# Kernel tuning notes

Measured on AMD Instinct MI355X. Metric: run time of the kernel, lower is better.

Reference implementation:

```python
import jax, jax.numpy as jnp
import numpy as np

B, S, D, L = 4, 2048, 1024, 4  # batch, seq_len, d_model, num_layers


def setup_inputs() -> dict:
    key = jax.random.key(0)
    ks = jax.random.split(key, 6)
    w = lambda k, shape: jax.random.normal(k, shape, jnp.float32) * 0.02
    return {
        "x": jax.random.normal(ks[0], (B, S, D), jnp.float32),
        # stacked per-layer parameters [L, ...]
        "Wkqv": w(ks[1], (L, D, 3 * D)),
        "Wm1": w(ks[2], (L, D, 2 * D)), "bm1": jnp.zeros((L, 2 * D), jnp.float32),
        "Wm2": w(ks[3], (L, D, D)), "bm2": jnp.zeros((L, D), jnp.float32),
        "gn_g": jnp.ones((L, D), jnp.float32), "gn_b": jnp.zeros((L, D), jnp.float32),
        "Wf1": w(ks[4], (L, D, 2 * D)), "bf1": jnp.zeros((L, 2 * D), jnp.float32),
        "Wf2": w(ks[5], (L, 2 * D, D)), "bf2": jnp.zeros((L, D), jnp.float32),
        "ln_g": jnp.ones((L, D), jnp.float32), "ln_b": jnp.zeros((L, D), jnp.float32),
    }


def _retention(x, wkqv):
    d = x.shape[-1]
    k, q, v = jnp.split(x @ wkqv, 3, axis=-1)            # each [B,S,D]
    qkt = jnp.einsum('bid,bjd->bij', q, k) / jnp.sqrt(jnp.float32(d))
    s = x.shape[1]
    row_norm = 1.0 + jnp.sqrt(jnp.arange(s, dtype=x.dtype))[None, :, None]
    r = jnp.tril(qkt) / row_norm                          # causal, per-row sqrt-index norm
    denom = jnp.clip(jnp.abs(r.sum(-1, keepdims=True)), 1.0, None)
    r = r / denom
    return jnp.einsum('bij,bjd->bid', r, v)


def _groupnorm1(y, g, b, eps=1e-5):
    # torch GroupNorm(1, D) on [B, D, S]: normalize over (D, S) per batch element
    mu = y.mean(axis=(1, 2), keepdims=True)
    var = y.var(axis=(1, 2), keepdims=True)
    return (y - mu) / jnp.sqrt(var + eps) * g + b


def _layernorm(y, g, b, eps=1e-5):
    mu = y.mean(-1, keepdims=True)
    var = y.var(-1, keepdims=True)
    return (y - mu) / jnp.sqrt(var + eps) * g + b


def reference(x, Wkqv, Wm1, bm1, Wm2, bm2, gn_g, gn_b, Wf1, bf1, Wf2, bf2, ln_g, ln_b):
    def block(h, p):
        wk, w1, b1, w2, b2, gg, gb, wf1, bf1_, wf2, bf2_, lg, lb = p
        r = _retention(h, wk)
        m = r @ w1 + b1
        a, gate = jnp.split(m, 2, axis=-1)                # SwiGLU
        m = (a * jax.nn.silu(gate)) @ w2 + b2
        m = _groupnorm1(m, gg, gb)
        y = m + h
        f = jax.nn.gelu(y @ wf1 + bf1_, approximate=False) @ wf2 + bf2_
        return _layernorm(f + y, lg, lb), None

    params = (Wkqv, Wm1, bm1, Wm2, bm2, gn_g, gn_b, Wf1, bf1, Wf2, bf2, ln_g, ln_b)
    out, _ = jax.lax.scan(block, x, params)
    return out
```

## Files before the change

kernel.cpp:

```cpp
#include <hip/hip_runtime.h>


constexpr int Bb = 4, Ss = 2048, Dd = 1024, Ll = 4;
constexpr int BSm = Bb * Ss;

typedef short bf16x8 __attribute__((ext_vector_type(8)));
typedef float f32x4  __attribute__((ext_vector_type(4)));
typedef unsigned short us;

__device__ __forceinline__ us bf16_rn(float x) {
    unsigned int u = __float_as_uint(x);
    u += 0x7FFFu + ((u >> 16) & 1u);
    return (us)(u >> 16);
}
__device__ __forceinline__ float bf2f(us h) {
    return __uint_as_float(((unsigned int)h) << 16);
}
__device__ __forceinline__ void fsplit(float v, us& h, us& l) {
    h = bf16_rn(v);
    l = bf16_rn(v - bf2f(h));
}

#define GLL(g, l) __builtin_amdgcn_global_load_lds( \
    (const __attribute__((address_space(1))) void*)(g), \
    (__attribute__((address_space(3))) void*)(l), 16, 0, 0)

#define MFMA(c, a, b) asm("v_mfma_f32_16x16x32_bf16 %0, %1, %2, %0" \
                          : "+v"(c) : "v"(a), "v"(b))

template<int OUT, bool HAS_BIAS, int ACT, bool CAUSAL, bool CK, bool ROWSCALE>
__global__ __launch_bounds__(256, 2) void gemm3(
    const us* __restrict__ Ahg, const us* __restrict__ Alg, int lda, long sA,
    const us* __restrict__ Bhg, const us* __restrict__ Blg, int ldb, long sB,
    const float* __restrict__ bias,
    float* __restrict__ Cf, us* __restrict__ Ch, us* __restrict__ Cl,
    int ldc, long sC,
    const float* __restrict__ drec, int K)
{
    if (CAUSAL && blockIdx.x > blockIdx.y) return;
    __shared__ us LAh[128 * 32], LAl[128 * 32], LBh[128 * 32], LBl[128 * 32];
    const int t = threadIdx.x, z = blockIdx.z;
    const int row0 = blockIdx.y * 128, col0 = blockIdx.x * 128;
    Ahg += (size_t)z * sA;  Alg += (size_t)z * sA;
    Bhg += (size_t)z * sB;  Blg += (size_t)z * sB;

    const int srow = t >> 2;
    const int scg  = ((t & 3) ^ ((t >> 3) & 3)) * 8;
    const us* pAh = Ahg + (size_t)(row0 + srow) * lda + scg;
    const us* pAl = Alg + (size_t)(row0 + srow) * lda + scg;
    const us* pBh = Bhg + (size_t)(col0 + srow) * ldb + scg;
    const us* pBl = Blg + (size_t)(col0 + srow) * ldb + scg;
    const size_t a64 = (size_t)64 * lda, b64 = (size_t)64 * ldb;
    const int wb = (t >> 6) * 1024;

    const int l  = t & 63, lr = l & 15, q = l >> 4;
    const int w  = t >> 6, wm = w >> 1, wn = w & 1;
    const int xq = (q ^ ((lr >> 1) & 3)) * 16;
    int offA[4], offB[4];
    #pragma unroll
    for (int m = 0; m < 4; ++m) offA[m] = (wm * 64 + m * 16 + lr) * 64 + xq;
    #pragma unroll
    for (int n = 0; n < 4; ++n) offB[n] = (wn * 64 + n * 16 + lr) * 64 + xq;

    f32x4 acc[4][4] = {};
    int Keff = K;
    if (CK) { int ke = row0 + 128; Keff = ke < K ? ke : K; }

    for (int k0 = 0; k0 < Keff; k0 += 32) {
        GLL(pAh + k0,       (char*)LAh + wb);
        GLL(pAh + k0 + a64, (char*)LAh + 4096 + wb);
        GLL(pAl + k0,       (char*)LAl + wb);
        GLL(pAl + k0 + a64, (char*)LAl + 4096 + wb);
        GLL(pBh + k0,       (char*)LBh + wb);
        GLL(pBh + k0 + b64, (char*)LBh + 4096 + wb);
        GLL(pBl + k0,       (char*)LBl + wb);
        GLL(pBl + k0 + b64, (char*)LBl + 4096 + wb);
        __syncthreads();
        bf16x8 ah[4], al4[4], bh[4], bl4[4];
        #pragma unroll
        for (int m = 0; m < 4; ++m) {
            ah[m]  = *reinterpret_cast<const bf16x8*>((const char*)LAh + offA[m]);
            al4[m] = *reinterpret_cast<const bf16x8*>((const char*)LAl + offA[m]);
        }
        #pragma unroll
        for (int n = 0; n < 4; ++n) {
            bh[n]  = *reinterpret_cast<const bf16x8*>((const char*)LBh + offB[n]);
            bl4[n] = *reinterpret_cast<const bf16x8*>((const char*)LBl + offB[n]);
        }
        #pragma unroll
        for (int m = 0; m < 4; ++m)
            #pragma unroll
            for (int n = 0; n < 4; ++n) {
                MFMA(acc[m][n], ah[m],  bh[n]);
                MFMA(acc[m][n], ah[m],  bl4[n]);
                MFMA(acc[m][n], al4[m], bh[n]);
            }
        __syncthreads();
    }

    const float* dz = drec + (size_t)z * Ss;
    #pragma unroll
    for (int n = 0; n < 4; ++n) {
        const int col = col0 + wn * 64 + n * 16 + lr;
        const float bv = HAS_BIAS ? bias[col] : 0.0f;
        #pragma unroll
        for (int m = 0; m < 4; ++m) {
            #pragma unroll
            for (int j = 0; j < 4; ++j) {
                const int row = row0 + wm * 64 + m * 16 + 4 * q + j;
                float v = acc[m][n][j] + bv;
                if (ACT == 1)
                    v = 0.5f * v * (1.0f + erff(v * 0.70710678118f));
                if (CAUSAL)
                    v = (col <= row)
                        ? v * (1.0f / (32.0f * (1.0f + sqrtf((float)row))))
                        : 0.0f;
                if (ROWSCALE) v *= dz[row];
                const size_t idx = (size_t)z * sC + (size_t)row * ldc + col;
                if (OUT == 0) {
                    Cf[idx] = v;
                } else {
                    us h_, l_;
                    fsplit(v, h_, l_);
                    Ch[idx] = h_;
                    Cl[idx] = l_;
                }
            }
        }
    }
}

__global__ __launch_bounds__(256) void split_k(
    const float* __restrict__ in, us* __restrict__ oh, us* __restrict__ ol)
{
    const size_t e = (size_t)blockIdx.x * 256 + threadIdx.x;
    float4 v = *reinterpret_cast<const float4*>(in + e * 4);
    ushort4 h4, l4;
    fsplit(v.x, h4.x, l4.x); fsplit(v.y, h4.y, l4.y);
    fsplit(v.z, h4.z, l4.z); fsplit(v.w, h4.w, l4.w);
    *reinterpret_cast<ushort4*>(oh + e * 4) = h4;
    *reinterpret_cast<ushort4*>(ol + e * 4) = l4;
}

__global__ __launch_bounds__(256) void tsplit_k(
    const float* __restrict__ in, long sin_,
    us* __restrict__ oh, us* __restrict__ ol, long sout, int H, int W)
{
    __shared__ float tile[32][33];
    const int z = blockIdx.z;
    in += (size_t)z * sin_;  oh += (size_t)z * sout;  ol += (size_t)z * sout;
    const int c0 = blockIdx.x * 32, r0 = blockIdx.y * 32;
    const int tr = threadIdx.x >> 3, tc = (threadIdx.x & 7) * 4;
    float4 v = *reinterpret_cast<const float4*>(in + (size_t)(r0 + tr) * W + c0 + tc);
    tile[tr][tc + 0] = v.x; tile[tr][tc + 1] = v.y;
    tile[tr][tc + 2] = v.z; tile[tr][tc + 3] = v.w;
    __syncthreads();
    ushort4 h4, l4;
    fsplit(tile[tc + 0][tr], h4.x, l4.x);
    fsplit(tile[tc + 1][tr], h4.y, l4.y);
    fsplit(tile[tc + 2][tr], h4.z, l4.z);
    fsplit(tile[tc + 3][tr], h4.w, l4.w);
    const size_t o = (size_t)(c0 + tr) * H + r0 + tc;
    *reinterpret_cast<ushort4*>(oh + o) = h4;
    *reinterpret_cast<ushort4*>(ol + o) = l4;
}

__global__ __launch_bounds__(256) void denom_k(
    const us* __restrict__ sph, const us* __restrict__ spl,
    float* __restrict__ drec)
{
    const int r = blockIdx.x, b = blockIdx.y, t = threadIdx.x;
    const us* ph = sph + ((size_t)b * Ss + r) * Ss;
    const us* pl = spl + ((size_t)b * Ss + r) * Ss;
    const int jmax = ((r >> 7) + 1) << 7;
    float s = 0.f;
    for (int j4 = t; j4 * 4 < jmax; j4 += 256) {
        ushort4 h = *reinterpret_cast<const ushort4*>(ph + j4 * 4);
        ushort4 lo = *reinterpret_cast<const ushort4*>(pl + j4 * 4);
        s += (bf2f(h.x) + bf2f(lo.x)) + (bf2f(h.y) + bf2f(lo.y))
           + (bf2f(h.z) + bf2f(lo.z)) + (bf2f(h.w) + bf2f(lo.w));
    }
    __shared__ float rs[256];
    rs[t] = s;
    __syncthreads();
    for (int off = 128; off > 0; off >>= 1) {
        if (t < off) rs[t] += rs[t + off];
        __syncthreads();
    }
    if (t == 0) drec[(size_t)b * Ss + r] = 1.0f / fmaxf(1.0f, fabsf(rs[0]));
}

__global__ __launch_bounds__(256) void swiglu_k(
    const float* __restrict__ m1, us* __restrict__ oh, us* __restrict__ ol)
{
    const size_t e = (size_t)blockIdx.x * 256 + threadIdx.x;
    const size_t row = e / (Dd / 4);
    const int c4 = (int)(e % (Dd / 4));
    const float* base = m1 + row * (2 * Dd);
    float4 a = *reinterpret_cast<const float4*>(base + c4 * 4);
    float4 g = *reinterpret_cast<const float4*>(base + Dd + c4 * 4);
    float o0 = a.x * (g.x / (1.f + expf(-g.x)));
    float o1 = a.y * (g.y / (1.f + expf(-g.y)));
    float o2 = a.z * (g.z / (1.f + expf(-g.z)));
    float o3 = a.w * (g.w / (1.f + expf(-g.w)));
    ushort4 h4, l4;
    fsplit(o0, h4.x, l4.x); fsplit(o1, h4.y, l4.y);
    fsplit(o2, h4.z, l4.z); fsplit(o3, h4.w, l4.w);
    const size_t o = row * Dd + c4 * 4;
    *reinterpret_cast<ushort4*>(oh + o) = h4;
    *reinterpret_cast<ushort4*>(ol + o) = l4;
}

__global__ __launch_bounds__(256) void gn_part_k(
    const float* __restrict__ m2, float* __restrict__ part)
{
    const int b = blockIdx.y, blk = blockIdx.x;
    const float* p = m2 + (size_t)b * Ss * Dd + (size_t)blk * 8192;
    float s = 0.f, ss = 0.f;
    for (int t = threadIdx.x; t < 2048; t += 256) {
        float4 v = *reinterpret_cast<const float4*>(p + (size_t)t * 4);
        s  += (v.x + v.y) + (v.z + v.w);
        ss += v.x * v.x + v.y * v.y + v.z * v.z + v.w * v.w;
    }
    __shared__ float rs[256], rss[256];
    rs[threadIdx.x] = s; rss[threadIdx.x] = ss;
    __syncthreads();
    for (int off = 128; off > 0; off >>= 1) {
        if (threadIdx.x < off) {
            rs[threadIdx.x]  += rs[threadIdx.x + off];
            rss[threadIdx.x] += rss[threadIdx.x + off];
        }
        __syncthreads();
    }
    if (threadIdx.x == 0) {
        part[(b * 256 + blk) * 2]     = rs[0];
        part[(b * 256 + blk) * 2 + 1] = rss[0];
    }
}

__global__ __launch_bounds__(256) void gn_final_k(
    const float* __restrict__ part, float* __restrict__ stats)
{
    const int b = blockIdx.x, t = threadIdx.x;
    float s  = part[(b * 256 + t) * 2];
    float ss = part[(b * 256 + t) * 2 + 1];
    __shared__ float rs[256], rss[256];
    rs[t] = s; rss[t] = ss;
    __syncthreads();
    for (int off = 128; off > 0; off >>= 1) {
        if (t < off) { rs[t] += rs[t + off]; rss[t] += rss[t + off]; }
        __syncthreads();
    }
    if (t == 0) {
        const float inv_n = 1.0f / (float)((size_t)Ss * Dd);
        float mean = rs[0] * inv_n;
        float var  = fmaxf(rss[0] * inv_n - mean * mean, 0.0f);
        stats[b * 2]     = mean;
        stats[b * 2 + 1] = rsqrtf(var + 1e-5f);
    }
}

__global__ __launch_bounds__(256) void gn_apply_k(
    const float* __restrict__ m2, const float* __restrict__ h,
    const float* __restrict__ g, const float* __restrict__ bta,
    const float* __restrict__ stats, float* __restrict__ y,
    us* __restrict__ yh, us* __restrict__ yl)
{
    const size_t e = (size_t)blockIdx.x * 256 + threadIdx.x;
    const int b  = (int)(e / ((size_t)Ss * Dd / 4));
    const int c4 = (int)(e % (Dd / 4));
    const float mean = stats[b * 2], istd = stats[b * 2 + 1];
    float4 m  = *reinterpret_cast<const float4*>(m2 + e * 4);
    float4 hh = *reinterpret_cast<const float4*>(h + e * 4);
    float4 g4 = *reinterpret_cast<const float4*>(g + c4 * 4);
    float4 b4 = *reinterpret_cast<const float4*>(bta + c4 * 4);
    float4 o;
    o.x = (m.x - mean) * istd * g4.x + b4.x + hh.x;
    o.y = (m.y - mean) * istd * g4.y + b4.y + hh.y;
    o.z = (m.z - mean) * istd * g4.z + b4.z + hh.z;
    o.w = (m.w - mean) * istd * g4.w + b4.w + hh.w;
    *reinterpret_cast<float4*>(y + e * 4) = o;
    ushort4 h4, l4;
    fsplit(o.x, h4.x, l4.x); fsplit(o.y, h4.y, l4.y);
    fsplit(o.z, h4.z, l4.z); fsplit(o.w, h4.w, l4.w);
    *reinterpret_cast<ushort4*>(yh + e * 4) = h4;
    *reinterpret_cast<ushort4*>(yl + e * 4) = l4;
}

template<bool SPLIT>
__global__ __launch_bounds__(256) void ln_k(
    const float* __restrict__ f2, const float* __restrict__ y,
    const float* __restrict__ g, const float* __restrict__ bta,
    float* __restrict__ out, us* __restrict__ oh, us* __restrict__ ol)
{
    const int row = blockIdx.x;
    const int t = threadIdx.x;
    float4 fv = *reinterpret_cast<const float4*>(f2 + (size_t)row * Dd + t * 4);
    float4 yv = *reinterpret_cast<const float4*>(y  + (size_t)row * Dd + t * 4);
    const float v0 = fv.x + yv.x, v1 = fv.y + yv.y;
    const float v2 = fv.z + yv.z, v3 = fv.w + yv.w;
    float s  = (v0 + v1) + (v2 + v3);
    float ss = v0 * v0 + v1 * v1 + v2 * v2 + v3 * v3;
    __shared__ float rs[256], rss[256];
    rs[t] = s; rss[t] = ss;
    __syncthreads();
    for (int off = 128; off > 0; off >>= 1) {
        if (t < off) { rs[t] += rs[t + off]; rss[t] += rss[t + off]; }
        __syncthreads();
    }
    const float mean = rs[0] * (1.0f / Dd);
    const float var  = fmaxf(rss[0] * (1.0f / Dd) - mean * mean, 0.0f);
    const float istd = rsqrtf(var + 1e-5f);
    float4 g4 = *reinterpret_cast<const float4*>(g + t * 4);
    float4 b4 = *reinterpret_cast<const float4*>(bta + t * 4);
    float4 o;
    o.x = (v0 - mean) * istd * g4.x + b4.x;
    o.y = (v1 - mean) * istd * g4.y + b4.y;
    o.z = (v2 - mean) * istd * g4.z + b4.z;
    o.w = (v3 - mean) * istd * g4.w + b4.w;
    *reinterpret_cast<float4*>(out + (size_t)row * Dd + t * 4) = o;
    if (SPLIT) {
        ushort4 h4, l4;
        fsplit(o.x, h4.x, l4.x); fsplit(o.y, h4.y, l4.y);
        fsplit(o.z, h4.z, l4.z); fsplit(o.w, h4.w, l4.w);
        const size_t e = (size_t)row * Dd + t * 4;
        *reinterpret_cast<ushort4*>(oh + e) = h4;
        *reinterpret_cast<ushort4*>(ol + e) = l4;
    }
}

extern "C" void kernel_launch(void* const* d_in, const int* in_sizes, int n_in,
                              void* d_out, int out_size, void* d_ws, size_t ws_size,
                              hipStream_t stream)
{
    const float* x    = (const float*)d_in[0];
    const float* Wkqv = (const float*)d_in[1];
    const float* Wm1  = (const float*)d_in[2];
    const float* bm1  = (const float*)d_in[3];
    const float* Wm2  = (const float*)d_in[4];
    const float* bm2  = (const float*)d_in[5];
    const float* gng  = (const float*)d_in[6];
    const float* gnb  = (const float*)d_in[7];
    const float* Wf1  = (const float*)d_in[8];
    const float* bf1  = (const float*)d_in[9];
    const float* Wf2  = (const float*)d_in[10];
    const float* bf2  = (const float*)d_in[11];
    const float* lng  = (const float*)d_in[12];
    const float* lnb  = (const float*)d_in[13];

    char* wsb = (char*)d_ws;
    const size_t MiB = 1024 * 1024;
    auto SL = [&](int i) { return wsb + (size_t)i * 16 * MiB; };

    float* hbuf   = (float*)SL(0);
    us* h_hi      = (us*)SL(2);
    us* h_lo      = (us*)SL(3);
    us* qk_hi     = (us*)SL(4);
    us* qk_lo     = (us*)SL(6);
    float* vbuf   = (float*)SL(8);
    us* WtA_hi    = (us*)SL(10);
    us* WtA_lo    = (us*)(SL(10) + 6 * MiB);
    us* vT_hi     = (us*)SL(2);
    us* vT_lo     = (us*)SL(3);
    us* sp_hi     = (us*)SL(8);
    us* sp_lo     = (us*)SL(10);
    float* drec   = (float*)SL(4);
    us* ret_hi    = (us*)SL(6);
    us* ret_lo    = (us*)SL(7);
    us* Wt1_hi    = (us*)SL(2);
    us* Wt1_lo    = (us*)(SL(2) + 4 * MiB);
    float* m1     = (float*)SL(8);
    us* sw_hi     = (us*)SL(4);
    us* sw_lo     = (us*)SL(5);
    us* Wt2_hi    = (us*)SL(2);
    us* Wt2_lo    = (us*)(SL(2) + 2 * MiB);
    float* m2     = (float*)SL(10);
    float* part   = (float*)SL(2);
    float* stats  = (float*)(SL(2) + 1 * MiB);
    float* ybuf   = (float*)SL(8);
    us* y_hi      = (us*)SL(4);
    us* y_lo      = (us*)SL(5);
    us* Wtf1_hi   = (us*)SL(6);
    us* Wtf1_lo   = (us*)(SL(6) + 4 * MiB);
    us* f1_hi     = (us*)SL(10);
    us* f1_lo     = (us*)SL(2);
    us* Wtf2_hi   = (us*)SL(6);
    us* Wtf2_lo   = (us*)(SL(6) + 4 * MiB);
    float* f2     = (float*)SL(4);

    for (int l = 0; l < Ll; ++l) {
        const float* h = (l == 0) ? x : hbuf;
        if (l == 0)
            split_k<<<8192, 256, 0, stream>>>(x, h_hi, h_lo);

        tsplit_k<<<dim3(3 * Dd / 32, Dd / 32, 1), 256, 0, stream>>>(
            Wkqv + (size_t)l * Dd * 3 * Dd, 0, WtA_hi, WtA_lo, 0, Dd, 3 * Dd);
        gemm3<1, false, 0, false, false, false><<<dim3(16, 64, 1), 256, 0, stream>>>(
            h_hi, h_lo, Dd, 0, WtA_hi, WtA_lo, Dd, 0, nullptr,
            nullptr, qk_hi, qk_lo, 2 * Dd, 0, drec, Dd);
        gemm3<0, false, 0, false, false, false><<<dim3(8, 64, 1), 256, 0, stream>>>(
            h_hi, h_lo, Dd, 0,
            WtA_hi + (size_t)2 * Dd * Dd, WtA_lo + (size_t)2 * Dd * Dd, Dd, 0,
            nullptr, vbuf, nullptr, nullptr, Dd, 0, drec, Dd);
        tsplit_k<<<dim3(Dd / 32, Ss / 32, Bb), 256, 0, stream>>>(
            vbuf, (long)Ss * Dd, vT_hi, vT_lo, (long)Dd * Ss, Ss, Dd);

        gemm3<1, false, 0, true, false, false><<<dim3(16, 16, Bb), 256, 0, stream>>>(
            qk_hi + Dd, qk_lo + Dd, 2 * Dd, (long)Ss * 2 * Dd,
            qk_hi,      qk_lo,      2 * Dd, (long)Ss * 2 * Dd,
            nullptr, nullptr, sp_hi, sp_lo, Ss, (long)Ss * Ss, drec, Dd);
        denom_k<<<dim3(Ss, Bb), 256, 0, stream>>>(sp_hi, sp_lo, drec);
        gemm3<1, false, 0, false, true, true><<<dim3(8, 16, Bb), 256, 0, stream>>>(
            sp_hi, sp_lo, Ss, (long)Ss * Ss,
            vT_hi, vT_lo, Ss, (long)Dd * Ss,
            nullptr, nullptr, ret_hi, ret_lo, Dd, (long)Ss * Dd, drec, Ss);

        tsplit_k<<<dim3(2 * Dd / 32, Dd / 32, 1), 256, 0, stream>>>(
            Wm1 + (size_t)l * Dd * 2 * Dd, 0, Wt1_hi, Wt1_lo, 0, Dd, 2 * Dd);
        gemm3<0, true, 0, false, false, false><<<dim3(16, 64, 1), 256, 0, stream>>>(
            ret_hi, ret_lo, Dd, 0, Wt1_hi, Wt1_lo, Dd, 0,
            bm1 + (size_t)l * 2 * Dd, m1, nullptr, nullptr, 2 * Dd, 0, drec, Dd);
        swiglu_k<<<8192, 256, 0, stream>>>(m1, sw_hi, sw_lo);
        tsplit_k<<<dim3(Dd / 32, Dd / 32, 1), 256, 0, stream>>>(
            Wm2 + (size_t)l * Dd * Dd, 0, Wt2_hi, Wt2_lo, 0, Dd, Dd);
        gemm3<0, true, 0, false, false, false><<<dim3(8, 64, 1), 256, 0, stream>>>(
            sw_hi, sw_lo, Dd, 0, Wt2_hi, Wt2_lo, Dd, 0,
            bm2 + (size_t)l * Dd, m2, nullptr, nullptr, Dd, 0, drec, Dd);

        gn_part_k<<<dim3(256, Bb), 256, 0, stream>>>(m2, part);
        gn_final_k<<<Bb, 256, 0, stream>>>(part, stats);
        gn_apply_k<<<8192, 256, 0, stream>>>(
            m2, h, gng + (size_t)l * Dd, gnb + (size_t)l * Dd, stats,
            ybuf, y_hi, y_lo);

        tsplit_k<<<dim3(2 * Dd / 32, Dd / 32, 1), 256, 0, stream>>>(
            Wf1 + (size_t)l * Dd * 2 * Dd, 0, Wtf1_hi, Wtf1_lo, 0, Dd, 2 * Dd);
        gemm3<1, true, 1, false, false, false><<<dim3(16, 64, 1), 256, 0, stream>>>(
            y_hi, y_lo, Dd, 0, Wtf1_hi, Wtf1_lo, Dd, 0,
            bf1 + (size_t)l * 2 * Dd,
            nullptr, f1_hi, f1_lo, 2 * Dd, 0, drec, Dd);
        tsplit_k<<<dim3(Dd / 32, 2 * Dd / 32, 1), 256, 0, stream>>>(
            Wf2 + (size_t)l * 2 * Dd * Dd, 0, Wtf2_hi, Wtf2_lo, 0, 2 * Dd, Dd);
        gemm3<0, true, 0, false, false, false><<<dim3(8, 64, 1), 256, 0, stream>>>(
            f1_hi, f1_lo, 2 * Dd, 0, Wtf2_hi, Wtf2_lo, 2 * Dd, 0,
            bf2 + (size_t)l * Dd, f2, nullptr, nullptr, Dd, 0, drec, 2 * Dd);

        if (l == Ll - 1)
            ln_k<false><<<BSm, 256, 0, stream>>>(
                f2, ybuf, lng + (size_t)l * Dd, lnb + (size_t)l * Dd,
                (float*)d_out, nullptr, nullptr);
        else
            ln_k<true><<<BSm, 256, 0, stream>>>(
                f2, ybuf, lng + (size_t)l * Dd, lnb + (size_t)l * Dd,
                hbuf, h_hi, h_lo);
    }
}
```

Baseline: 3.612 ms.

## Enlarge GEMM tiles to 256xBN with 512 threads and double-buffered LDS prefetch

The split-bf16 GEMM is rebuilt to use 256-row tiles (256 or 128 columns) with 8 waves per block. It adds a two-stage LDS double buffer, fed by global_load_lds prefetches two K-steps ahead and guarded by explicit vmcnt waits and barriers. The LDS layout changes to a k-chunk-major arrangement without the XOR swizzle, and MFMA issue runs at raised wave priority. The aim is to increase operand reuse per LDS load and to hide global memory latency behind compute. In exchange it brings higher register and LDS pressure, fewer blocks per launch, coarser causal-tile granularity (the denominator kernel's range is widened to match), and possible LDS bank conflicts from dropping the swizzle.

```diff
diff --git a/kernel.cpp b/kernel.cpp
--- a/kernel.cpp
+++ b/kernel.cpp
@@ -28,8 +28,8 @@
 #define MFMA(c, a, b) asm("v_mfma_f32_16x16x32_bf16 %0, %1, %2, %0" \
                           : "+v"(c) : "v"(a), "v"(b))
 
-template<int OUT, bool HAS_BIAS, int ACT, bool CAUSAL, bool CK, bool ROWSCALE>
-__global__ __launch_bounds__(256, 2) void gemm3(
+template<int BN, int OUT, bool HAS_BIAS, int ACT, bool CAUSAL, bool CK, bool ROWSCALE>
+__global__ __launch_bounds__(512, 2) void gemm3(
     const us* __restrict__ Ahg, const us* __restrict__ Alg, int lda, long sA,
     const us* __restrict__ Bhg, const us* __restrict__ Blg, int ldb, long sB,
     const float* __restrict__ bias,
@@ -37,77 +37,120 @@
     int ldc, long sC,
     const float* __restrict__ drec, int K)
 {
+    constexpr int BM = 256;
+    constexpr int CW = BN / 4;
+    constexpr int NR = CW / 16;
+    constexpr int ASLOT = 4 * BM;
+    constexpr int BSLOT = 4 * BN;
+    constexpr int ABYTES = 4 * ASLOT * 16;
+    constexpr int BBYTES = 4 * BSLOT * 16;
+    __shared__ char lds[ABYTES + BBYTES];
+
     if (CAUSAL && blockIdx.x > blockIdx.y) return;
-    __shared__ us LAh[128 * 32], LAl[128 * 32], LBh[128 * 32], LBl[128 * 32];
     const int t = threadIdx.x, z = blockIdx.z;
-    const int row0 = blockIdx.y * 128, col0 = blockIdx.x * 128;
+    const int row0 = blockIdx.y * BM, col0 = blockIdx.x * BN;
     Ahg += (size_t)z * sA;  Alg += (size_t)z * sA;
     Bhg += (size_t)z * sB;  Blg += (size_t)z * sB;
 
-    const int srow = t >> 2;
-    const int scg  = ((t & 3) ^ ((t >> 3) & 3)) * 8;
-    const us* pAh = Ahg + (size_t)(row0 + srow) * lda + scg;
-    const us* pAl = Alg + (size_t)(row0 + srow) * lda + scg;
-    const us* pBh = Bhg + (size_t)(col0 + srow) * ldb + scg;
-    const us* pBl = Blg + (size_t)(col0 + srow) * ldb + scg;
-    const size_t a64 = (size_t)64 * lda, b64 = (size_t)64 * ldb;
-    const int wb = (t >> 6) * 1024;
-
-    const int l  = t & 63, lr = l & 15, q = l >> 4;
-    const int w  = t >> 6, wm = w >> 1, wn = w & 1;
-    const int xq = (q ^ ((lr >> 1) & 3)) * 16;
-    int offA[4], offB[4];
+    const us* pAh = Ahg + (size_t)(row0 + (t & 255)) * lda + (t >> 8) * 8;
+    const us* pAl = Alg + (size_t)(row0 + (t & 255)) * lda + (t >> 8) * 8;
+    const us* pBh; const us* pBl;
+    if constexpr (BN == 256) {
+        pBh = Bhg + (size_t)(col0 + (t & 255)) * ldb + (t >> 8) * 8;
+        pBl = Blg + (size_t)(col0 + (t & 255)) * ldb + (t >> 8) * 8;
+    } else {
+        pBh = Bhg + (size_t)(col0 + (t & 127)) * ldb + (t >> 7) * 8;
+        pBl = Blg + (size_t)(col0 + (t & 127)) * ldb + (t >> 7) * 8;
+    }
+    const int wub = (t >> 6) * 1024;
+
+    auto stage = [&](int buf, int k0) {
+        char* aH = lds + (size_t)(buf * 2 + 0) * (ASLOT * 16) + wub;
+        char* aL = lds + (size_t)(buf * 2 + 1) * (ASLOT * 16) + wub;
+        char* bH = lds + ABYTES + (size_t)(buf * 2 + 0) * (BSLOT * 16) + wub;
+        char* bL = lds + ABYTES + (size_t)(buf * 2 + 1) * (BSLOT * 16) + wub;
+        GLL(pAh + k0,      aH);
+        GLL(pAh + k0 + 16, aH + 8192);
+        GLL(pAl + k0,      aL);
+        GLL(pAl + k0 + 16, aL + 8192);
+        GLL(pBh + k0,      bH);
+        GLL(pBl + k0,      bL);
+        if constexpr (BN == 256) {
+            GLL(pBh + k0 + 16, bH + 8192);
+            GLL(pBl + k0 + 16, bL + 8192);
+        }
+    };
+
+    const int ln = t & 63, lr = ln & 15, q = ln >> 4;
+    const int w  = t >> 6, wm = w >> 2, wn = w & 3;
+    int offA[8], offB[NR];
     #pragma unroll
-    for (int m = 0; m < 4; ++m) offA[m] = (wm * 64 + m * 16 + lr) * 64 + xq;
+    for (int m = 0; m < 8; ++m)
+        offA[m] = ((q * BM) + (wm * 128 + m * 16 + lr)) * 16;
     #pragma unroll
-    for (int n = 0; n < 4; ++n) offB[n] = (wn * 64 + n * 16 + lr) * 64 + xq;
-
-    f32x4 acc[4][4] = {};
+    for (int n = 0; n < NR; ++n)
+        offB[n] = ((q * BN) + (wn * CW + n * 16 + lr)) * 16;
+
+    f32x4 acc[8][NR] = {};
+
     int Keff = K;
-    if (CK) { int ke = row0 + 128; Keff = ke < K ? ke : K; }
-
-    for (int k0 = 0; k0 < Keff; k0 += 32) {
-        GLL(pAh + k0,       (char*)LAh + wb);
-        GLL(pAh + k0 + a64, (char*)LAh + 4096 + wb);
-        GLL(pAl + k0,       (char*)LAl + wb);
-        GLL(pAl + k0 + a64, (char*)LAl + 4096 + wb);
-        GLL(pBh + k0,       (char*)LBh + wb);
-        GLL(pBh + k0 + b64, (char*)LBh + 4096 + wb);
-        GLL(pBl + k0,       (char*)LBl + wb);
-        GLL(pBl + k0 + b64, (char*)LBl + 4096 + wb);
-        __syncthreads();
-        bf16x8 ah[4], al4[4], bh[4], bl4[4];
+    if (CK) { int ke = row0 + BM; Keff = ke < K ? ke : K; }
+    const int NT = Keff >> 5;
+
+    stage(0, 0);
+    stage(1, 32);
+    for (int kt = 0; kt < NT; ++kt) {
+        const int buf = kt & 1;
+        if (kt < NT - 1) {
+            if constexpr (BN == 256)
+                asm volatile("s_waitcnt vmcnt(8)" ::: "memory");
+            else
+                asm volatile("s_waitcnt vmcnt(6)" ::: "memory");
+        } else {
+            asm volatile("s_waitcnt vmcnt(0)" ::: "memory");
+        }
+        __builtin_amdgcn_sched_barrier(0);
+        __builtin_amdgcn_s_barrier();
+        __builtin_amdgcn_sched_barrier(0);
+        const char* aH = lds + (size_t)(buf * 2 + 0) * (ASLOT * 16);
+        const char* aL = lds + (size_t)(buf * 2 + 1) * (ASLOT * 16);
+        const char* bH = lds + ABYTES + (size_t)(buf * 2 + 0) * (BSLOT * 16);
+        const char* bL = lds + ABYTES + (size_t)(buf * 2 + 1) * (BSLOT * 16);
+        bf16x8 ah[8], al8[8];
         #pragma unroll
-        for (int m = 0; m < 4; ++m) {
-            ah[m]  = *reinterpret_cast<const bf16x8*>((const char*)LAh + offA[m]);
-            al4[m] = *reinterpret_cast<const bf16x8*>((const char*)LAl + offA[m]);
+        for (int m = 0; m < 8; ++m) {
+            ah[m]  = *reinterpret_cast<const bf16x8*>(aH + offA[m]);
+            al8[m] = *reinterpret_cast<const bf16x8*>(aL + offA[m]);
         }
+        __builtin_amdgcn_s_setprio(1);
         #pragma unroll
-        for (int n = 0; n < 4; ++n) {
-            bh[n]  = *reinterpret_cast<const bf16x8*>((const char*)LBh + offB[n]);
-            bl4[n] = *reinterpret_cast<const bf16x8*>((const char*)LBl + offB[n]);
+        for (int n = 0; n < NR; ++n) {
+            bf16x8 bh = *reinterpret_cast<const bf16x8*>(bH + offB[n]);
+            bf16x8 bl = *reinterpret_cast<const bf16x8*>(bL + offB[n]);
+            #pragma unroll
+            for (int m = 0; m < 8; ++m) {
+                MFMA(acc[m][n], ah[m],  bh);
+                MFMA(acc[m][n], ah[m],  bl);
+                MFMA(acc[m][n], al8[m], bh);
+            }
         }
-        #pragma unroll
-        for (int m = 0; m < 4; ++m)
-            #pragma unroll
-            for (int n = 0; n < 4; ++n) {
-                MFMA(acc[m][n], ah[m],  bh[n]);
-                MFMA(acc[m][n], ah[m],  bl4[n]);
-                MFMA(acc[m][n], al4[m], bh[n]);
-            }
-        __syncthreads();
+        __builtin_amdgcn_s_setprio(0);
+        __builtin_amdgcn_sched_barrier(0);
+        __builtin_amdgcn_s_barrier();
+        __builtin_amdgcn_sched_barrier(0);
+        if (kt + 2 < NT) stage(buf, (kt + 2) * 32);
     }
 
     const float* dz = drec + (size_t)z * Ss;
     #pragma unroll
-    for (int n = 0; n < 4; ++n) {
-        const int col = col0 + wn * 64 + n * 16 + lr;
+    for (int n = 0; n < NR; ++n) {
+        const int col = col0 + wn * CW + n * 16 + lr;
         const float bv = HAS_BIAS ? bias[col] : 0.0f;
         #pragma unroll
-        for (int m = 0; m < 4; ++m) {
+        for (int m = 0; m < 8; ++m) {
             #pragma unroll
             for (int j = 0; j < 4; ++j) {
-                const int row = row0 + wm * 64 + m * 16 + 4 * q + j;
+                const int row = row0 + wm * 128 + m * 16 + 4 * q + j;
                 float v = acc[m][n][j] + bv;
                 if (ACT == 1)
                     v = 0.5f * v * (1.0f + erff(v * 0.70710678118f));
@@ -172,7 +215,7 @@
     const int r = blockIdx.x, b = blockIdx.y, t = threadIdx.x;
     const us* ph = sph + ((size_t)b * Ss + r) * Ss;
     const us* pl = spl + ((size_t)b * Ss + r) * Ss;
-    const int jmax = ((r >> 7) + 1) << 7;
+    const int jmax = ((r >> 8) + 1) << 8;
     float s = 0.f;
     for (int j4 = t; j4 * 4 < jmax; j4 += 256) {
         ushort4 h = *reinterpret_cast<const ushort4*>(ph + j4 * 4);
@@ -395,35 +438,35 @@
 
         tsplit_k<<<dim3(3 * Dd / 32, Dd / 32, 1), 256, 0, stream>>>(
             Wkqv + (size_t)l * Dd * 3 * Dd, 0, WtA_hi, WtA_lo, 0, Dd, 3 * Dd);
-        gemm3<1, false, 0, false, false, false><<<dim3(16, 64, 1), 256, 0, stream>>>(
+        gemm3<256, 1, false, 0, false, false, false><<<dim3(8, 32, 1), 512, 0, stream>>>(
             h_hi, h_lo, Dd, 0, WtA_hi, WtA_lo, Dd, 0, nullptr,
             nullptr, qk_hi, qk_lo, 2 * Dd, 0, drec, Dd);
-        gemm3<0, false, 0, false, false, false><<<dim3(8, 64, 1), 256, 0, stream>>>(
+        gemm3<128, 0, false, 0, false, false, false><<<dim3(8, 32, 1), 512, 0, stream>>>(
             h_hi, h_lo, Dd, 0,
             WtA_hi + (size_t)2 * Dd * Dd, WtA_lo + (size_t)2 * Dd * Dd, Dd, 0,
             nullptr, vbuf, nullptr, nullptr, Dd, 0, drec, Dd);
         tsplit_k<<<dim3(Dd / 32, Ss / 32, Bb), 256, 0, stream>>>(
             vbuf, (long)Ss * Dd, vT_hi, vT_lo, (long)Dd * Ss, Ss, Dd);
 
-        gemm3<1, false, 0, true, false, false><<<dim3(16, 16, Bb), 256, 0, stream>>>(
+        gemm3<256, 1, false, 0, true, false, false><<<dim3(8, 8, Bb), 512, 0, stream>>>(
             qk_hi + Dd, qk_lo + Dd, 2 * Dd, (long)Ss * 2 * Dd,
             qk_hi,      qk_lo,      2 * Dd, (long)Ss * 2 * Dd,
             nullptr, nullptr, sp_hi, sp_lo, Ss, (long)Ss * Ss, drec, Dd);
         denom_k<<<dim3(Ss, Bb), 256, 0, stream>>>(sp_hi, sp_lo, drec);
-        gemm3<1, false, 0, false, true, true><<<dim3(8, 16, Bb), 256, 0, stream>>>(
+        gemm3<128, 1, false, 0, false, true, true><<<dim3(8, 8, Bb), 512, 0, stream>>>(
             sp_hi, sp_lo, Ss, (long)Ss * Ss,
             vT_hi, vT_lo, Ss, (long)Dd * Ss,
             nullptr, nullptr, ret_hi, ret_lo, Dd, (long)Ss * Dd, drec, Ss);
 
         tsplit_k<<<dim3(2 * Dd / 32, Dd / 32, 1), 256, 0, stream>>>(
             Wm1 + (size_t)l * Dd * 2 * Dd, 0, Wt1_hi, Wt1_lo, 0, Dd, 2 * Dd);
-        gemm3<0, true, 0, false, false, false><<<dim3(16, 64, 1), 256, 0, stream>>>(
+        gemm3<256, 0, true, 0, false, false, false><<<dim3(8, 32, 1), 512, 0, stream>>>(
             ret_hi, ret_lo, Dd, 0, Wt1_hi, Wt1_lo, Dd, 0,
             bm1 + (size_t)l * 2 * Dd, m1, nullptr, nullptr, 2 * Dd, 0, drec, Dd);
         swiglu_k<<<8192, 256, 0, stream>>>(m1, sw_hi, sw_lo);
         tsplit_k<<<dim3(Dd / 32, Dd / 32, 1), 256, 0, stream>>>(
             Wm2 + (size_t)l * Dd * Dd, 0, Wt2_hi, Wt2_lo, 0, Dd, Dd);
-        gemm3<0, true, 0, false, false, false><<<dim3(8, 64, 1), 256, 0, stream>>>(
+        gemm3<128, 0, true, 0, false, false, false><<<dim3(8, 32, 1), 512, 0, stream>>>(
             sw_hi, sw_lo, Dd, 0, Wt2_hi, Wt2_lo, Dd, 0,
             bm2 + (size_t)l * Dd, m2, nullptr, nullptr, Dd, 0, drec, Dd);
 
@@ -435,13 +478,13 @@
 
         tsplit_k<<<dim3(2 * Dd / 32, Dd / 32, 1), 256, 0, stream>>>(
             Wf1 + (size_t)l * Dd * 2 * Dd, 0, Wtf1_hi, Wtf1_lo, 0, Dd, 2 * Dd);
-        gemm3<1, true, 1, false, false, false><<<dim3(16, 64, 1), 256, 0, stream>>>(
+        gemm3<256, 1, true, 1, false, false, false><<<dim3(8, 32, 1), 512, 0, stream>>>(
             y_hi, y_lo, Dd, 0, Wtf1_hi, Wtf1_lo, Dd, 0,
             bf1 + (size_t)l * 2 * Dd,
             nullptr, f1_hi, f1_lo, 2 * Dd, 0, drec, Dd);
         tsplit_k<<<dim3(Dd / 32, 2 * Dd / 32, 1), 256, 0, stream>>>(
             Wf2 + (size_t)l * 2 * Dd * Dd, 0, Wtf2_hi, Wtf2_lo, 0, 2 * Dd, Dd);
-        gemm3<0, true, 0, false, false, false><<<dim3(8, 64, 1), 256, 0, stream>>>(
+        gemm3<128, 0, true, 0, false, false, false><<<dim3(8, 32, 1), 512, 0, stream>>>(
             f1_hi, f1_lo, 2 * Dd, 0, Wtf2_hi, Wtf2_lo, 2 * Dd, 0,
             bf2 + (size_t)l * Dd, f2, nullptr, nullptr, Dd, 0, drec, 2 * Dd);
 
```

Measured after the change: 5.166 ms. +43.0%, slower.

## Double-buffer GEMM LDS tiles and switch MFMA to compiler builtin

Applied to the files above, without the earlier changes.

The split-bf16 GEMM now uses two LDS buffers, so the global-to-LDS load of the next K tile is issued before the MFMAs on the current tile. This is meant to hide load latency and drop one barrier per iteration. The LDS layout changes from an XOR swizzle to a k-chunk-major layout, and the inline-asm MFMA becomes the builtin with a reordered issue sequence so the compiler can schedule it. LDS use doubles to 64KB per block, which may limit occupancy at 2 blocks per CU. The new unswizzled layout may also cause bank conflicts.

```diff
diff --git a/kernel.cpp b/kernel.cpp
--- a/kernel.cpp
+++ b/kernel.cpp
@@ -25,8 +25,7 @@
     (const __attribute__((address_space(1))) void*)(g), \
     (__attribute__((address_space(3))) void*)(l), 16, 0, 0)
 
-#define MFMA(c, a, b) asm("v_mfma_f32_16x16x32_bf16 %0, %1, %2, %0" \
-                          : "+v"(c) : "v"(a), "v"(b))
+#define MFMA16(a, b, c) __builtin_amdgcn_mfma_f32_16x16x32_bf16(a, b, c, 0, 0, 0)
 
 template<int OUT, bool HAS_BIAS, int ACT, bool CAUSAL, bool CK, bool ROWSCALE>
 __global__ __launch_bounds__(256, 2) void gemm3(
@@ -37,64 +36,77 @@
     int ldc, long sC,
     const float* __restrict__ drec, int K)
 {
+    constexpr int PB = 8192;
+    __shared__ __align__(16) char lds[2 * 4 * PB];
+
     if (CAUSAL && blockIdx.x > blockIdx.y) return;
-    __shared__ us LAh[128 * 32], LAl[128 * 32], LBh[128 * 32], LBl[128 * 32];
     const int t = threadIdx.x, z = blockIdx.z;
     const int row0 = blockIdx.y * 128, col0 = blockIdx.x * 128;
     Ahg += (size_t)z * sA;  Alg += (size_t)z * sA;
     Bhg += (size_t)z * sB;  Blg += (size_t)z * sB;
 
-    const int srow = t >> 2;
-    const int scg  = ((t & 3) ^ ((t >> 3) & 3)) * 8;
-    const us* pAh = Ahg + (size_t)(row0 + srow) * lda + scg;
-    const us* pAl = Alg + (size_t)(row0 + srow) * lda + scg;
-    const us* pBh = Bhg + (size_t)(col0 + srow) * ldb + scg;
-    const us* pBl = Blg + (size_t)(col0 + srow) * ldb + scg;
-    const size_t a64 = (size_t)64 * lda, b64 = (size_t)64 * ldb;
-    const int wb = (t >> 6) * 1024;
-
-    const int l  = t & 63, lr = l & 15, q = l >> 4;
+    const int aoff = (row0 + (t & 127)) * lda + (t >> 7) * 8;
+    const int boff = (col0 + (t & 127)) * ldb + (t >> 7) * 8;
+    const int wub  = (t >> 6) * 1024;
+
+    auto stage = [&](int kt) {
+        const int k0 = kt * 32;
+        char* base = lds + (kt & 1) * (4 * PB) + wub;
+        const us* gAh = Ahg + aoff + k0;
+        const us* gAl = Alg + aoff + k0;
+        const us* gBh = Bhg + boff + k0;
+        const us* gBl = Blg + boff + k0;
+        GLL(gAh,      base + 0 * PB);
+        GLL(gAh + 16, base + 0 * PB + 4096);
+        GLL(gAl,      base + 1 * PB);
+        GLL(gAl + 16, base + 1 * PB + 4096);
+        GLL(gBh,      base + 2 * PB);
+        GLL(gBh + 16, base + 2 * PB + 4096);
+        GLL(gBl,      base + 3 * PB);
+        GLL(gBl + 16, base + 3 * PB + 4096);
+    };
+
+    const int ln = t & 63, lr = ln & 15, q = ln >> 4;
     const int w  = t >> 6, wm = w >> 1, wn = w & 1;
-    const int xq = (q ^ ((lr >> 1) & 3)) * 16;
     int offA[4], offB[4];
     #pragma unroll
-    for (int m = 0; m < 4; ++m) offA[m] = (wm * 64 + m * 16 + lr) * 64 + xq;
+    for (int m = 0; m < 4; ++m)
+        offA[m] = ((q * 128) + (wm * 64 + m * 16 + lr)) * 16;
     #pragma unroll
-    for (int n = 0; n < 4; ++n) offB[n] = (wn * 64 + n * 16 + lr) * 64 + xq;
+    for (int n = 0; n < 4; ++n)
+        offB[n] = ((q * 128) + (wn * 64 + n * 16 + lr)) * 16;
 
     f32x4 acc[4][4] = {};
+
     int Keff = K;
     if (CK) { int ke = row0 + 128; Keff = ke < K ? ke : K; }
-
-    for (int k0 = 0; k0 < Keff; k0 += 32) {
-        GLL(pAh + k0,       (char*)LAh + wb);
-        GLL(pAh + k0 + a64, (char*)LAh + 4096 + wb);
-        GLL(pAl + k0,       (char*)LAl + wb);
-        GLL(pAl + k0 + a64, (char*)LAl + 4096 + wb);
-        GLL(pBh + k0,       (char*)LBh + wb);
-        GLL(pBh + k0 + b64, (char*)LBh + 4096 + wb);
-        GLL(pBl + k0,       (char*)LBl + wb);
-        GLL(pBl + k0 + b64, (char*)LBl + 4096 + wb);
-        __syncthreads();
-        bf16x8 ah[4], al4[4], bh[4], bl4[4];
+    const int NT = Keff >> 5;
+
+    stage(0);
+    __syncthreads();
+    for (int kt = 0; kt < NT; ++kt) {
+        if (kt + 1 < NT) stage(kt + 1);
+        const char* base = lds + (kt & 1) * (4 * PB);
+        bf16x8 ah[4], al8[4], bh[4], bl8[4];
         #pragma unroll
         for (int m = 0; m < 4; ++m) {
-            ah[m]  = *reinterpret_cast<const bf16x8*>((const char*)LAh + offA[m]);
-            al4[m] = *reinterpret_cast<const bf16x8*>((const char*)LAl + offA[m]);
+            ah[m]  = *reinterpret_cast<const bf16x8*>(base + 0 * PB + offA[m]);
+            al8[m] = *reinterpret_cast<const bf16x8*>(base + 1 * PB + offA[m]);
         }
         #pragma unroll
         for (int n = 0; n < 4; ++n) {
-            bh[n]  = *reinterpret_cast<const bf16x8*>((const char*)LBh + offB[n]);
-            bl4[n] = *reinterpret_cast<const bf16x8*>((const char*)LBl + offB[n]);
+            bh[n]  = *reinterpret_cast<const bf16x8*>(base + 2 * PB + offB[n]);
+            bl8[n] = *reinterpret_cast<const bf16x8*>(base + 3 * PB + offB[n]);
         }
         #pragma unroll
-        for (int m = 0; m < 4; ++m)
+        for (int n = 0; n < 4; ++n) {
             #pragma unroll
-            for (int n = 0; n < 4; ++n) {
-                MFMA(acc[m][n], ah[m],  bh[n]);
-                MFMA(acc[m][n], ah[m],  bl4[n]);
-                MFMA(acc[m][n], al4[m], bh[n]);
-            }
+            for (int m = 0; m < 4; ++m) acc[m][n] = MFMA16(ah[m],  bh[n],  acc[m][n]);
+            #pragma unroll
+            for (int m = 0; m < 4; ++m) acc[m][n] = MFMA16(ah[m],  bl8[n], acc[m][n]);
+            #pragma unroll
+            for (int m = 0; m < 4; ++m) acc[m][n] = MFMA16(al8[m], bh[n],  acc[m][n]);
+        }
         __syncthreads();
     }
 
```

New measurement: 4.996 ms. 1.38x slower.

## Double-buffer LDS tiles in split-bf16 GEMM and use MFMA builtin

Applied to the files above, without the earlier changes.

The GEMM main loop now uses two 32 KB LDS buffers. The next K-tile is issued with global_load_lds right after a single barrier, while MFMAs run on the current tile, so global-memory latency overlaps compute and one barrier per iteration is removed. Inline-asm MFMA is replaced by the compiler builtin, with loops reordered by n, which lets the compiler schedule the instructions and track hazards. The cost is doubled LDS per block (64 KB), which could limit occupancy at two blocks per CU.

```diff
diff --git a/kernel.cpp b/kernel.cpp
--- a/kernel.cpp
+++ b/kernel.cpp
@@ -25,8 +25,7 @@
     (const __attribute__((address_space(1))) void*)(g), \
     (__attribute__((address_space(3))) void*)(l), 16, 0, 0)
 
-#define MFMA(c, a, b) asm("v_mfma_f32_16x16x32_bf16 %0, %1, %2, %0" \
-                          : "+v"(c) : "v"(a), "v"(b))
+#define MFMA16(a, b, c) __builtin_amdgcn_mfma_f32_16x16x32_bf16(a, b, c, 0, 0, 0)
 
 template<int OUT, bool HAS_BIAS, int ACT, bool CAUSAL, bool CK, bool ROWSCALE>
 __global__ __launch_bounds__(256, 2) void gemm3(
@@ -37,8 +36,9 @@
     int ldc, long sC,
     const float* __restrict__ drec, int K)
 {
+    __shared__ __align__(16) char lds[2 * 32768];
+
     if (CAUSAL && blockIdx.x > blockIdx.y) return;
-    __shared__ us LAh[128 * 32], LAl[128 * 32], LBh[128 * 32], LBl[128 * 32];
     const int t = threadIdx.x, z = blockIdx.z;
     const int row0 = blockIdx.y * 128, col0 = blockIdx.x * 128;
     Ahg += (size_t)z * sA;  Alg += (size_t)z * sA;
@@ -53,7 +53,20 @@
     const size_t a64 = (size_t)64 * lda, b64 = (size_t)64 * ldb;
     const int wb = (t >> 6) * 1024;
 
-    const int l  = t & 63, lr = l & 15, q = l >> 4;
+    auto stage = [&](int kt) {
+        const int k0 = kt * 32;
+        char* base = lds + (kt & 1) * 32768 + wb;
+        GLL(pAh + k0,       base + 0 * 8192);
+        GLL(pAh + k0 + a64, base + 0 * 8192 + 4096);
+        GLL(pAl + k0,       base + 1 * 8192);
+        GLL(pAl + k0 + a64, base + 1 * 8192 + 4096);
+        GLL(pBh + k0,       base + 2 * 8192);
+        GLL(pBh + k0 + b64, base + 2 * 8192 + 4096);
+        GLL(pBl + k0,       base + 3 * 8192);
+        GLL(pBl + k0 + b64, base + 3 * 8192 + 4096);
+    };
+
+    const int ln = t & 63, lr = ln & 15, q = ln >> 4;
     const int w  = t >> 6, wm = w >> 1, wn = w & 1;
     const int xq = (q ^ ((lr >> 1) & 3)) * 16;
     int offA[4], offB[4];
@@ -63,39 +76,36 @@
     for (int n = 0; n < 4; ++n) offB[n] = (wn * 64 + n * 16 + lr) * 64 + xq;
 
     f32x4 acc[4][4] = {};
+
     int Keff = K;
     if (CK) { int ke = row0 + 128; Keff = ke < K ? ke : K; }
-
-    for (int k0 = 0; k0 < Keff; k0 += 32) {
-        GLL(pAh + k0,       (char*)LAh + wb);
-        GLL(pAh + k0 + a64, (char*)LAh + 4096 + wb);
-        GLL(pAl + k0,       (char*)LAl + wb);
-        GLL(pAl + k0 + a64, (char*)LAl + 4096 + wb);
-        GLL(pBh + k0,       (char*)LBh + wb);
-        GLL(pBh + k0 + b64, (char*)LBh + 4096 + wb);
-        GLL(pBl + k0,       (char*)LBl + wb);
-        GLL(pBl + k0 + b64, (char*)LBl + 4096 + wb);
+    const int NT = Keff >> 5;
+
+    stage(0);
+    for (int kt = 0; kt < NT; ++kt) {
         __syncthreads();
-        bf16x8 ah[4], al4[4], bh[4], bl4[4];
+        if (kt + 1 < NT) stage(kt + 1);
+        const char* base = lds + (kt & 1) * 32768;
+        bf16x8 ah[4], al8[4], bh[4], bl8[4];
         #pragma unroll
         for (int m = 0; m < 4; ++m) {
-            ah[m]  = *reinterpret_cast<const bf16x8*>((const char*)LAh + offA[m]);
-            al4[m] = *reinterpret_cast<const bf16x8*>((const char*)LAl + offA[m]);
+            ah[m]  = *reinterpret_cast<const bf16x8*>(base + 0 * 8192 + offA[m]);
+            al8[m] = *reinterpret_cast<const bf16x8*>(base + 1 * 8192 + offA[m]);
         }
         #pragma unroll
         for (int n = 0; n < 4; ++n) {
-            bh[n]  = *reinterpret_cast<const bf16x8*>((const char*)LBh + offB[n]);
-            bl4[n] = *reinterpret_cast<const bf16x8*>((const char*)LBl + offB[n]);
+            bh[n]  = *reinterpret_cast<const bf16x8*>(base + 2 * 8192 + offB[n]);
+            bl8[n] = *reinterpret_cast<const bf16x8*>(base + 3 * 8192 + offB[n]);
         }
         #pragma unroll
-        for (int m = 0; m < 4; ++m)
+        for (int n = 0; n < 4; ++n) {
             #pragma unroll
-            for (int n = 0; n < 4; ++n) {
-                MFMA(acc[m][n], ah[m],  bh[n]);
-                MFMA(acc[m][n], ah[m],  bl4[n]);
-                MFMA(acc[m][n], al4[m], bh[n]);
-            }
-        __syncthreads();
+            for (int m = 0; m < 4; ++m) acc[m][n] = MFMA16(ah[m],  bh[n],  acc[m][n]);
+            #pragma unroll
+            for (int m = 0; m < 4; ++m) acc[m][n] = MFMA16(ah[m],  bl8[n], acc[m][n]);
+            #pragma unroll
+            for (int m = 0; m < 4; ++m) acc[m][n] = MFMA16(al8[m], bh[n],  acc[m][n]);
+        }
     }
 
     const float* dz = drec + (size_t)z * Ss;
```

Result: faster. 3.503 ms (-3.0%).
